# Kernel tuning notes

Measured on AMD Instinct MI355X. Metric: run time of the kernel, lower is better.

## Reference

```python
import jax, jax.numpy as jnp
import numpy as np

B, N, C, K = 2, 8192, 128, 16

def _mlp2(h, W1, b1, W2, b2):
    return jax.nn.relu(h @ W1 + b1) @ W2 + b2

def setup_inputs() -> dict:
    key = jax.random.key(0)
    ks = jax.random.split(key, 20)
    s = lambda d: 1.0 / np.sqrt(d)
    inp = {
        "x": jax.random.normal(ks[0], (B, N, C), jnp.float32),
        "position": jax.random.normal(ks[1], (B, N, 3), jnp.float32),
        "Wq": jax.random.normal(ks[2], (C, C), jnp.float32) * s(C),
        "bq": jnp.zeros((C,), jnp.float32),
        "Wk": jax.random.normal(ks[3], (C, C), jnp.float32) * s(C),
        "bk": jnp.zeros((C,), jnp.float32),
        "Wv": jax.random.normal(ks[4], (C, C), jnp.float32) * s(C),
        "bv": jnp.zeros((C,), jnp.float32),
        "Wp1": jax.random.normal(ks[5], (3, C), jnp.float32) * s(3),
        "bp1": jnp.zeros((C,), jnp.float32),
        "Wp2": jax.random.normal(ks[6], (C, C), jnp.float32) * s(C),
        "bp2": jnp.zeros((C,), jnp.float32),
        "Wg1": jax.random.normal(ks[7], (C, C), jnp.float32) * s(C),
        "bg1": jnp.zeros((C,), jnp.float32),
        "Wg2": jax.random.normal(ks[8], (C, C), jnp.float32) * s(C),
        "bg2": jnp.zeros((C,), jnp.float32),
    }
    return inp

def reference(x, position, Wq, bq, Wk, bk, Wv, bv, Wp1, bp1, Wp2, bp2, Wg1, bg1, Wg2, bg2):
    # kNN via squared pairwise distances (monotone in cdist, same topk indices)
    p2 = jnp.sum(position * position, axis=-1)                       # (B,N)
    d2 = p2[:, :, None] + p2[:, None, :] - 2.0 * jnp.einsum("bnd,bmd->bnm", position, position)
    _, idx = jax.lax.top_k(-d2, K)                                    # (B,N,K) nearest (incl self)

    gather = jax.vmap(lambda arr, i: arr[i])                          # per-batch fancy gather
    neighbors = gather(x, idx)                                        # (B,N,K,C)
    pos_nb = gather(position, idx)                                    # (B,N,K,3)

    q = x @ Wq + bq                                                   # (B,N,C)
    k = neighbors @ Wk + bk                                           # (B,N,K,C)
    v = neighbors @ Wv + bv                                           # (B,N,K,C)

    # positional MLP only at gathered pairs (same math as all-pairs-then-gather)
    rel = position[:, :, None, :] - pos_nb                            # (B,N,K,3)
    pe = _mlp2(rel, Wp1, bp1, Wp2, bp2)                               # (B,N,K,C)

    scale = 1.0 / jnp.sqrt(jnp.float32(C))
    attn = (q[:, :, None, :] - k + pe) * scale
    attn = _mlp2(attn, Wg1, bg1, Wg2, bg2)
    attn = jax.nn.softmax(attn, axis=2)                               # softmax over K neighbors
    out = jnp.sum(attn * (v + pe), axis=2)                            # (B,N,C)
    return out
```

## Files before the change

kernel.cpp:

```cpp
#include <hip/hip_runtime.h>
#include <hip/hip_bf16.h>
#include <stdint.h>

#define NPTS 8192
#define CDIM 128
#define KNNK 16
#define WELEMF 16384
#define SCALE 0.08838834764831845f
#define FLDS_BYTES 74752
#define GRES 16
#define NCELL (GRES*GRES*GRES)

typedef __attribute__((ext_vector_type(4))) float f32x4;
typedef __attribute__((ext_vector_type(8))) short s16x8;

__device__ __forceinline__ unsigned short to_bf16(float f){
  union { __hip_bfloat16 h; unsigned short u; } v;
  v.h = __float2bfloat16(f);
  return v.u;
}

__device__ __forceinline__ s16x8 cvt8(const float* p){
  float4 lo = *(const float4*)p;
  float4 hi = *(const float4*)(p + 4);
  s16x8 f;
  f[0]=(short)to_bf16(lo.x); f[1]=(short)to_bf16(lo.y);
  f[2]=(short)to_bf16(lo.z); f[3]=(short)to_bf16(lo.w);
  f[4]=(short)to_bf16(hi.x); f[5]=(short)to_bf16(hi.y);
  f[6]=(short)to_bf16(hi.z); f[7]=(short)to_bf16(hi.w);
  return f;
}

__device__ __forceinline__ unsigned mapf_u(unsigned s){
  return s ^ (0x80000000u | (unsigned)(((int)s) >> 31));
}
__device__ __forceinline__ float unmapf_u(unsigned u){
  unsigned r = (u & 0x80000000u) ? (u ^ 0x80000000u) : ~u;
  return __uint_as_float(r);
}

__global__ __launch_bounds__(256) void zero_init_kernel(int* __restrict__ counts,
                                                        unsigned* __restrict__ bbox)
{
  int t = blockIdx.x*256 + threadIdx.x;
  if (t < 2*NCELL) counts[t] = 0;
  if (t < 12) bbox[t] = ((t % 6) < 3) ? 0xFFFFFFFFu : 0u;
}

__global__ __launch_bounds__(256) void prep_kernel(
    const float* __restrict__ Wq, const float* __restrict__ Wk,
    const float* __restrict__ Wv, const float* __restrict__ Wp2,
    const float* __restrict__ Wg1, const float* __restrict__ Wg2,
    const float* __restrict__ pos,
    unsigned short* __restrict__ wt, float4* __restrict__ pos4,
    unsigned* __restrict__ bbox)
{
  int t = blockIdx.x*256 + threadIdx.x;
  if (t < 6*WELEMF){
    int w = t >> 14, f = t & (WELEMF-1);
    int i = f & 7, ln = (f >> 3) & 63, kkct = f >> 9;
    int kk = kkct & 3, ct = kkct >> 2;
    int kdim = kk*32 + (ln >> 4)*8 + i, col = ct*16 + (ln & 15);
    const float* src = (w==0)?Wq:(w==1)?Wk:(w==2)?Wv:(w==3)?Wp2:(w==4)?Wg1:Wg2;
    float v = src[kdim*CDIM + col];
    if (w == 1) v = -v;
    wt[t] = to_bf16(v);
  } else {
    int m = t - 6*WELEMF;
    float xx = pos[m*3+0], yy = pos[m*3+1], zz = pos[m*3+2];
    float p2 = __fadd_rn(__fadd_rn(__fmul_rn(xx,xx), __fmul_rn(yy,yy)), __fmul_rn(zz,zz));
    pos4[m] = make_float4(xx, yy, zz, p2);
    unsigned mnx = mapf_u(__float_as_uint(xx)), mny = mapf_u(__float_as_uint(yy)), mnz = mapf_u(__float_as_uint(zz));
    unsigned mxx = mnx, mxy = mny, mxz = mnz;
#pragma unroll
    for (int off = 1; off < 64; off <<= 1){
      mnx = min(mnx, (unsigned)__shfl_xor((int)mnx, off));
      mny = min(mny, (unsigned)__shfl_xor((int)mny, off));
      mnz = min(mnz, (unsigned)__shfl_xor((int)mnz, off));
      mxx = max(mxx, (unsigned)__shfl_xor((int)mxx, off));
      mxy = max(mxy, (unsigned)__shfl_xor((int)mxy, off));
      mxz = max(mxz, (unsigned)__shfl_xor((int)mxz, off));
    }
    if ((threadIdx.x & 63) == 0){
      int b = m >> 13;
      atomicMin(&bbox[b*6+0], mnx); atomicMin(&bbox[b*6+1], mny); atomicMin(&bbox[b*6+2], mnz);
      atomicMax(&bbox[b*6+3], mxx); atomicMax(&bbox[b*6+4], mxy); atomicMax(&bbox[b*6+5], mxz);
    }
  }
}

__global__ __launch_bounds__(256) void bin_count_kernel(
    const float4* __restrict__ pos4, const unsigned* __restrict__ bbox,
    int* __restrict__ counts, int* __restrict__ cellId)
{
  int m = blockIdx.x*256 + threadIdx.x;
  int b = m >> 13;
  float4 p = pos4[m];
  float lox = unmapf_u(bbox[b*6+0]), loy = unmapf_u(bbox[b*6+1]), loz = unmapf_u(bbox[b*6+2]);
  float hix = unmapf_u(bbox[b*6+3]), hiy = unmapf_u(bbox[b*6+4]), hiz = unmapf_u(bbox[b*6+5]);
  int ix = min(GRES-1, max(0, (int)((p.x - lox) * ((float)GRES/(hix-lox)))));
  int iy = min(GRES-1, max(0, (int)((p.y - loy) * ((float)GRES/(hiy-loy)))));
  int iz = min(GRES-1, max(0, (int)((p.z - loz) * ((float)GRES/(hiz-loz)))));
  int cid = (iz*GRES + iy)*GRES + ix;
  cellId[m] = cid;
  atomicAdd(&counts[b*NCELL + cid], 1);
}

__global__ __launch_bounds__(1024) void scan_kernel(
    const int* __restrict__ counts, int* __restrict__ starts, int* __restrict__ cursor)
{
  __shared__ int part[1024];
  int b = blockIdx.x, t = threadIdx.x;
  const int* c = counts + b*NCELL;
  int* s = starts + b*(NCELL+1);
  int* cur = cursor + b*NCELL;
  int base = t*4, sum = 0;
  for (int i = 0; i < 4; ++i) sum += c[base+i];
  part[t] = sum; __syncthreads();
  for (int off = 1; off < 1024; off <<= 1){
    int v = (t >= off) ? part[t-off] : 0;
    __syncthreads();
    part[t] += v;
    __syncthreads();
  }
  int run = (t > 0) ? part[t-1] : 0;
  for (int i = 0; i < 4; ++i){ int cc = c[base+i]; s[base+i] = run; cur[base+i] = run; run += cc; }
  if (t == 1023) s[NCELL] = run;
}

__global__ __launch_bounds__(256) void scatter_kernel(
    const float4* __restrict__ pos4, const int* __restrict__ cellId,
    int* __restrict__ cursor, float4* __restrict__ spos4)
{
  int m = blockIdx.x*256 + threadIdx.x;
  int b = m >> 13;
  float4 p = pos4[m];
  int dst = atomicAdd(&cursor[b*NCELL + cellId[m]], 1);
  spos4[(b<<13) + dst] = make_float4(p.x, p.y, p.z, __uint_as_float((unsigned)(m & (NPTS-1))));
}

__global__ __launch_bounds__(256) void knn_grid_kernel(
    const float4* __restrict__ spos4, const int* __restrict__ starts,
    const unsigned* __restrict__ bbox, int* __restrict__ idxout)
{
  const int tid = threadIdx.x, lane = tid & 63;
  const int g = blockIdx.x*4 + (tid >> 6);
  const int b = g >> 13, n = g & (NPTS-1);
  const float4* sp = spos4 + ((size_t)b<<13);
  const int*    st = starts + b*(NCELL+1);

  const float4 q4 = sp[n];
  const int orig = __float_as_int(q4.w);
  const float qx = q4.x, qy = q4.y, qz = q4.z;
  const float q2 = __fadd_rn(__fadd_rn(__fmul_rn(qx,qx), __fmul_rn(qy,qy)), __fmul_rn(qz,qz));

  float lox = unmapf_u(bbox[b*6+0]), loy = unmapf_u(bbox[b*6+1]), loz = unmapf_u(bbox[b*6+2]);
  float hix = unmapf_u(bbox[b*6+3]), hiy = unmapf_u(bbox[b*6+4]), hiz = unmapf_u(bbox[b*6+5]);
  float cwx = (hix-lox)*(1.0f/GRES), cwy = (hiy-loy)*(1.0f/GRES), cwz = (hiz-loz)*(1.0f/GRES);
  int cx = min(GRES-1, max(0, (int)((qx - lox) * ((float)GRES/(hix-lox)))));
  int cy = min(GRES-1, max(0, (int)((qy - loy) * ((float)GRES/(hiy-loy)))));
  int cz = min(GRES-1, max(0, (int)((qz - loz) * ((float)GRES/(hiz-loz)))));

  unsigned khi = 0xFFFFFFFFu, klo = 0xFFFFFFFFu;
  float Tf = __builtin_inff();

  auto insert = [&](unsigned ihi, unsigned ilo){
    unsigned phi = (unsigned)__builtin_amdgcn_update_dpp(0, (int)khi, 0x111, 0xF, 0xF, false);
    unsigned plo = (unsigned)__builtin_amdgcn_update_dpp(0, (int)klo, 0x111, 0xF, 0xF, false);
    bool gt  = (khi > ihi) || (khi == ihi && klo > ilo);
    bool pgt = ((lane & 15) != 0) && ((phi > ihi) || (phi == ihi && plo > ilo));
    khi = gt ? (pgt ? phi : ihi) : khi;
    klo = gt ? (pgt ? plo : ilo) : klo;
  };
  auto updT = [&](){
    unsigned t15 = (unsigned)__builtin_amdgcn_readlane((int)khi, 15);
    Tf = (t15 >= 0xFF800000u) ? __builtin_inff() : unmapf_u(t15);
  };

  for (int R = 1; R <= GRES-1; ++R){
    const bool first = (R == 1);
    const int per = 8*R, w1 = 2*R-1;
    const int ntask = first ? 9 : (per + 2*w1*w1);
    for (int tb = 0; tb < ntask; tb += 64){
      int t = tb + lane;
      int dy = 0, dz = 0, gx0 = 0, gx1 = -1;
      bool valid = t < ntask;
      if (first){
        if (valid){ dy = t % 3 - 1; dz = t / 3 - 1; }
        gx0 = max(cx-1, 0); gx1 = min(cx+1, GRES-1);
      } else if (valid){
        if (t < per){
          int s2 = 2*(2*R+1);
          if (t < s2){ dz = (t < 2*R+1) ? -R : R; dy = t % (2*R+1) - R; }
          else { int u = t - s2; dy = (u & 1) ? R : -R; dz = (u >> 1) - (R-1); }
          gx0 = max(cx-R, 0); gx1 = min(cx+R, GRES-1);
        } else {
          int i = t - per, ri = i >> 1;
          dy = ri % w1 - (R-1); dz = ri / w1 - (R-1);
          int gx = cx + ((i & 1) ? R : -R);
          gx0 = gx; gx1 = gx;
          valid = gx >= 0 && gx <= GRES-1;
        }
      }
      int gy = cy + dy, gz = cz + dz;
      valid = valid && gy >= 0 && gy < GRES && gz >= 0 && gz < GRES && gx0 <= gx1;
      int s0 = 0, s1 = 0;
      if (valid){ int cb = (gz*GRES + gy)*GRES; s0 = st[cb + gx0]; s1 = st[cb + gx1 + 1]; }
      unsigned long long cm = __ballot(valid && (s1 > s0));
      while (cm){
        int sl = (int)__builtin_ctzll(cm); cm &= cm - 1;
        int cs = __builtin_amdgcn_readlane(s0, sl);
        int ce = __builtin_amdgcn_readlane(s1, sl);
        for (int p0 = cs; p0 < ce; p0 += 64){
          int mm = p0 + lane;
          bool v = mm < ce;
          float4 c = v ? sp[mm] : make_float4(0.f,0.f,0.f,0.f);
          float c2  = __fadd_rn(__fadd_rn(__fmul_rn(c.x,c.x), __fmul_rn(c.y,c.y)), __fmul_rn(c.z,c.z));
          float dot = __builtin_fmaf(c.z, qz, __builtin_fmaf(c.y, qy, __fmul_rn(c.x, qx)));
          float d2  = __fsub_rn(__fadd_rn(q2, c2), __fadd_rn(dot, dot));
          int oi = __float_as_int(c.w);
          bool ins = v && (d2 <= Tf);
          unsigned long long im = __ballot(ins);
          if (im){
            while (im){
              int s = (int)__builtin_ctzll(im); im &= im - 1;
              unsigned dvb = (unsigned)__builtin_amdgcn_readlane((int)__float_as_uint(d2), s);
              int ov = __builtin_amdgcn_readlane(oi, s);
              insert(mapf_u(dvb), (unsigned)ov);
            }
            updT();
          }
        }
      }
    }
    const float big = 1e30f;
    float dxlo = (cx-R <= 0)      ? big : (qx - (lox + (float)(cx-R)*cwx));
    float dxhi = (cx+R >= GRES-1) ? big : ((lox + (float)(cx+R+1)*cwx) - qx);
    float dylo = (cy-R <= 0)      ? big : (qy - (loy + (float)(cy-R)*cwy));
    float dyhi = (cy+R >= GRES-1) ? big : ((loy + (float)(cy+R+1)*cwy) - qy);
    float dzlo = (cz-R <= 0)      ? big : (qz - (loz + (float)(cz-R)*cwz));
    float dzhi = (cz+R >= GRES-1) ? big : ((loz + (float)(cz+R+1)*cwz) - qz);
    float dmin = fminf(fminf(fminf(dxlo,dxhi), fminf(dylo,dyhi)), fminf(dzlo,dzhi));
    if (dmin >= 1e29f) break;
    dmin = fmaxf(dmin, 0.0f);
    float dmin2 = dmin*dmin;
    if (Tf + 1e-4f + Tf*1e-5f < dmin2) break;
  }
  if (lane < KNNK) idxout[(((size_t)b<<13) + orig)*KNNK + lane] = (int)klo;
}

__global__ __launch_bounds__(256, 2) void fused_kernel(
    const float* __restrict__ x, const float* __restrict__ pos,
    const float* __restrict__ bq, const float* __restrict__ bk,
    const float* __restrict__ bv, const float* __restrict__ Wp1,
    const float* __restrict__ bp1, const float* __restrict__ bp2,
    const float* __restrict__ bg1, const float* __restrict__ bg2,
    const int* __restrict__ idxws, const unsigned short* __restrict__ wt,
    float* __restrict__ out)
{
  extern __shared__ char smem[];
  char* Sbase = smem;
  char* Tbase = smem + 32768;
  float* blds = (float*)(smem + 65536);
  float* q_lds = (float*)(smem + 70656);

  const int tid = threadIdx.x;
  const int lane = tid & 63, w = tid >> 6;
  const int r = lane & 15, grp = lane >> 4;
  const int pbase = blockIdx.x * 8;
  const int b = pbase >> 13;

  auto gll = [&](int s, char* dst){
#pragma unroll
    for (int k = 0; k < 8; ++k){
      int c = w*8 + k;
      unsigned short* g = const_cast<unsigned short*>(wt) + (size_t)s*WELEMF + c*512 + lane*8;
      __builtin_amdgcn_global_load_lds(
        (const __attribute__((address_space(1))) void*)g,
        (__attribute__((address_space(3))) void*)(dst + c*1024), 16, 0, 0);
    }
  };
  auto ldS = [&](int ct, int kk) -> s16x8 {
    return *(const s16x8*)&((unsigned short*)Sbase)[((ct*4 + kk)*64 + lane)*8];
  };
  auto ldT = [&](int ct, int kk) -> s16x8 {
    return *(const s16x8*)&((unsigned short*)Tbase)[((ct*4 + kk)*64 + lane)*8];
  };

  gll(0, Sbase);
  gll(3, Tbase);

  for (int e = tid; e < 1280; e += 256){
    float v;
    if      (e < 128)  v = bq[e];
    else if (e < 256)  v = bk[e-128];
    else if (e < 384)  v = bv[e-256];
    else if (e < 512)  v = bp2[e-384];
    else if (e < 640)  v = bg1[e-512];
    else if (e < 768)  v = bg2[e-640];
    else if (e < 896)  v = bp1[e-768];
    else               v = Wp1[e-896];
    blds[e] = v;
  }
  int nbr[2]; float relx[2], rely[2], relz[2];
#pragma unroll
  for (int j = 0; j < 2; ++j){
    int gp = pbase + w*2 + j;
    nbr[j] = idxws[(size_t)gp*KNNK + r];
    const float* pq = pos + (size_t)gp*3;
    const float* pn = pos + ((size_t)b*NPTS + nbr[j])*3;
    relx[j] = pq[0]-pn[0]; rely[j] = pq[1]-pn[1]; relz[j] = pq[2]-pn[2];
  }
  s16x8 qa[4];
  {
    const float* xr = x + (size_t)(pbase + (r & 7))*CDIM;
#pragma unroll
    for (int kk = 0; kk < 4; ++kk) qa[kk] = cvt8(xr + kk*32 + grp*8);
  }
  __syncthreads();

  {
    f32x4 qacc[2] = { {0.f,0.f,0.f,0.f}, {0.f,0.f,0.f,0.f} };
#pragma unroll
    for (int c2 = 0; c2 < 2; ++c2){
      int ct = w*2 + c2;
#pragma unroll
      for (int kk = 0; kk < 4; ++kk)
        qacc[c2] = __builtin_amdgcn_mfma_f32_16x16x32_bf16(qa[kk], ldS(ct,kk), qacc[c2], 0,0,0);
    }
#pragma unroll
    for (int c2 = 0; c2 < 2; ++c2){
      int col = (w*2+c2)*16 + r;
#pragma unroll
      for (int jj = 0; jj < 4; ++jj){
        int row = grp*4 + jj;
        if (row < 8) q_lds[row*CDIM + col] = qacc[c2][jj] + blds[col];
      }
    }
  }
  s16x8 pf[2][4];
#pragma unroll
  for (int j = 0; j < 2; ++j)
#pragma unroll
    for (int kk = 0; kk < 4; ++kk){
      s16x8 f;
#pragma unroll
      for (int i = 0; i < 8; ++i){
        int kc = kk*32 + grp*8 + i;
        float s = relx[j]*blds[896+kc] + rely[j]*blds[1024+kc] + relz[j]*blds[1152+kc] + blds[768+kc];
        f[i] = (short)to_bf16(fmaxf(s, 0.f));
      }
      pf[j][kk] = f;
    }
  __syncthreads();
  gll(1, Sbase);

  f32x4 at[2][8], av[2][8];
#pragma unroll
  for (int j=0;j<2;++j)
#pragma unroll
    for (int ct=0;ct<8;++ct) at[j][ct] = (f32x4){0.f,0.f,0.f,0.f};
#pragma unroll
  for (int ct=0;ct<8;++ct)
#pragma unroll
    for (int kk=0;kk<4;++kk){
      s16x8 bw = ldT(ct,kk);
#pragma unroll
      for (int j=0;j<2;++j)
        at[j][ct] = __builtin_amdgcn_mfma_f32_16x16x32_bf16(pf[j][kk], bw, at[j][ct], 0,0,0);
    }
  s16x8 nf[2][4];
#pragma unroll
  for (int j=0;j<2;++j)
#pragma unroll
    for (int kk=0;kk<4;++kk)
      nf[j][kk] = cvt8(x + ((size_t)b*NPTS + nbr[j])*CDIM + kk*32 + grp*8);

  __syncthreads();
  gll(2, Tbase);
#pragma unroll
  for (int j=0;j<2;++j)
#pragma unroll
    for (int ct=0;ct<8;++ct) av[j][ct] = at[j][ct];
#pragma unroll
  for (int ct=0;ct<8;++ct)
#pragma unroll
    for (int kk=0;kk<4;++kk){
      s16x8 bw = ldS(ct,kk);
#pragma unroll
      for (int j=0;j<2;++j) at[j][ct] = __builtin_amdgcn_mfma_f32_16x16x32_bf16(nf[j][kk], bw, at[j][ct], 0,0,0);
    }
  __syncthreads();
  gll(4, Sbase);
#pragma unroll
  for (int ct=0;ct<8;++ct)
#pragma unroll
    for (int kk=0;kk<4;++kk){
      s16x8 bw = ldT(ct,kk);
#pragma unroll
      for (int j=0;j<2;++j) av[j][ct] = __builtin_amdgcn_mfma_f32_16x16x32_bf16(nf[j][kk], bw, av[j][ct], 0,0,0);
    }
#pragma unroll
  for (int j=0;j<2;++j){
    int prow = (w*2+j)*CDIM;
#pragma unroll
    for (int ct=0;ct<8;++ct){
      int col = ct*16+r;
      float add = q_lds[prow+col] + blds[384+col] - blds[128+col];
#pragma unroll
      for (int jj=0;jj<4;++jj) at[j][ct][jj] = (at[j][ct][jj] + add)*SCALE;
    }
  }
  __syncthreads();

#pragma unroll
  for (int j=0;j<2;++j){
    unsigned short* tj = (unsigned short*)Tbase + (w*2+j)*2048;
#pragma unroll
    for (int ct=0;ct<8;++ct){
      int base = (ct>>1)*512 + ((ct&1)*2 + (r>>3))*128 + (r&7);
#pragma unroll
      for (int jj=0;jj<4;++jj)
        tj[base + (grp*4+jj)*8] = to_bf16(at[j][ct][jj]);
    }
  }
  s16x8 tf[2][4];
#pragma unroll
  for (int j=0;j<2;++j){
    const unsigned short* tj = (const unsigned short*)Tbase + (w*2+j)*2048;
#pragma unroll
    for (int kk=0;kk<4;++kk)
      tf[j][kk] = *(const s16x8*)&tj[(kk*64 + lane)*8];
  }
  f32x4 hacc[2][8];
#pragma unroll
  for (int j=0;j<2;++j)
#pragma unroll
    for (int ct=0;ct<8;++ct) hacc[j][ct] = (f32x4){0.f,0.f,0.f,0.f};
#pragma unroll
  for (int ct=0;ct<8;++ct)
#pragma unroll
    for (int kk=0;kk<4;++kk){
      s16x8 bw = ldS(ct,kk);
#pragma unroll
      for (int j=0;j<2;++j)
        hacc[j][ct] = __builtin_amdgcn_mfma_f32_16x16x32_bf16(tf[j][kk], bw, hacc[j][ct], 0,0,0);
    }
  __syncthreads();
  gll(5, Sbase);
#pragma unroll
  for (int j=0;j<2;++j){
    unsigned short* tj = (unsigned short*)Tbase + (w*2+j)*2048;
#pragma unroll
    for (int ct=0;ct<8;++ct){
      int base = (ct>>1)*512 + ((ct&1)*2 + (r>>3))*128 + (r&7);
      int col = ct*16+r; float bb = blds[512+col];
#pragma unroll
      for (int jj=0;jj<4;++jj)
        tj[base + (grp*4+jj)*8] = to_bf16(fmaxf(hacc[j][ct][jj]+bb, 0.f));
    }
  }
  s16x8 hf[2][4];
#pragma unroll
  for (int j=0;j<2;++j){
    const unsigned short* tj = (const unsigned short*)Tbase + (w*2+j)*2048;
#pragma unroll
    for (int kk=0;kk<4;++kk)
      hf[j][kk] = *(const s16x8*)&tj[(kk*64 + lane)*8];
  }
  __syncthreads();
  f32x4 gacc[2][8];
#pragma unroll
  for (int j=0;j<2;++j)
#pragma unroll
    for (int ct=0;ct<8;++ct) gacc[j][ct] = (f32x4){0.f,0.f,0.f,0.f};
#pragma unroll
  for (int ct=0;ct<8;++ct)
#pragma unroll
    for (int kk=0;kk<4;++kk){
      s16x8 bw = ldS(ct,kk);
#pragma unroll
      for (int j=0;j<2;++j)
        gacc[j][ct] = __builtin_amdgcn_mfma_f32_16x16x32_bf16(hf[j][kk], bw, gacc[j][ct], 0,0,0);
    }
#pragma unroll
  for (int j=0;j<2;++j){
#pragma unroll
    for (int ct=0;ct<8;++ct){
      int col = ct*16+r;
      float gb = blds[640+col];
      float g0v = gacc[j][ct][0]+gb, g1v = gacc[j][ct][1]+gb;
      float g2v = gacc[j][ct][2]+gb, g3v = gacc[j][ct][3]+gb;
      float mx = fmaxf(fmaxf(g0v,g1v), fmaxf(g2v,g3v));
      mx = fmaxf(mx, __shfl_xor(mx,16));
      mx = fmaxf(mx, __shfl_xor(mx,32));
      float e0=__expf(g0v-mx), e1=__expf(g1v-mx), e2=__expf(g2v-mx), e3=__expf(g3v-mx);
      float vb = blds[256+col] + blds[384+col];
      float ss = e0+e1+e2+e3;
      float oo = e0*(av[j][ct][0]+vb) + e1*(av[j][ct][1]+vb)
               + e2*(av[j][ct][2]+vb) + e3*(av[j][ct][3]+vb);
      ss += __shfl_xor(ss,16); ss += __shfl_xor(ss,32);
      oo += __shfl_xor(oo,16); oo += __shfl_xor(oo,32);
      if (grp == 0) out[(size_t)(pbase + w*2 + j)*CDIM + col] = oo/ss;
    }
  }
}

extern "C" void kernel_launch(void* const* d_in, const int* in_sizes, int n_in,
                              void* d_out, int out_size, void* d_ws, size_t ws_size,
                              hipStream_t stream)
{
  const float* x    = (const float*)d_in[0];
  const float* pos  = (const float*)d_in[1];
  const float* Wq   = (const float*)d_in[2];
  const float* bq   = (const float*)d_in[3];
  const float* Wk   = (const float*)d_in[4];
  const float* bk   = (const float*)d_in[5];
  const float* Wv   = (const float*)d_in[6];
  const float* bv   = (const float*)d_in[7];
  const float* Wp1  = (const float*)d_in[8];
  const float* bp1  = (const float*)d_in[9];
  const float* Wp2  = (const float*)d_in[10];
  const float* bp2  = (const float*)d_in[11];
  const float* Wg1  = (const float*)d_in[12];
  const float* bg1  = (const float*)d_in[13];
  const float* Wg2  = (const float*)d_in[14];
  const float* bg2  = (const float*)d_in[15];
  float* out = (float*)d_out;

  char* ws = (char*)d_ws;
  int*            idxs   = (int*)ws;
  unsigned short* wt     = (unsigned short*)(ws + 1048576);
  float4*         pos4   = (float4*)(ws + 1257472);
  float4*         spos4  = (float4*)(ws + 1519616);
  int*            cellId = (int*)(ws + 1847296);
  int*            counts = (int*)(ws + 1912832);
  int*            starts = (int*)(ws + 2174976);
  int*            cursor = (int*)(ws + 2437376);
  unsigned*       bbox   = (unsigned*)(ws + 2699520);

  hipFuncSetAttribute((const void*)fused_kernel,
                      hipFuncAttributeMaxDynamicSharedMemorySize, FLDS_BYTES);

  zero_init_kernel<<<32, 256, 0, stream>>>(counts, bbox);
  prep_kernel<<<448, 256, 0, stream>>>(Wq, Wk, Wv, Wp2, Wg1, Wg2, pos, wt, pos4, bbox);
  bin_count_kernel<<<64, 256, 0, stream>>>(pos4, bbox, counts, cellId);
  scan_kernel<<<2, 1024, 0, stream>>>(counts, starts, cursor);
  scatter_kernel<<<64, 256, 0, stream>>>(pos4, cellId, cursor, spos4);
  knn_grid_kernel<<<4096, 256, 0, stream>>>(spos4, starts, bbox, idxs);
  fused_kernel<<<2048, 256, FLDS_BYTES, stream>>>(x, pos, bq, bk, bv, Wp1, bp1, bp2,
                                                  bg1, bg2, idxs, wt, out);
}
```

Baseline: 219.1 us.

## Process four kNN queries per wavefront using 16-lane subgroups

The grid kNN kernel now handles four query points per 64-lane wavefront, each on a 16-lane subgroup, instead of one query per wavefront. Ballots are masked per subgroup, readlane becomes shuffles, and the wave exits only once every subgroup has finished its search. Launched blocks drop by four times. This targets the many idle lanes in scans of small cells and in the serial insert loop, but adds divergence between subgroups whose searches differ in length, and each subgroup scans candidates only 16 at a time.

After: 211.4 us. 3.5% less time.

```diff
diff --git a/kernel.cpp b/kernel.cpp
--- a/kernel.cpp
+++ b/kernel.cpp
@@ -144,7 +144,9 @@
     const unsigned* __restrict__ bbox, int* __restrict__ idxout)
 {
   const int tid = threadIdx.x, lane = tid & 63;
-  const int g = blockIdx.x*4 + (tid >> 6);
+  const int sub = lane >> 4, sl = lane & 15, gbase = sub*16;
+  const int w = tid >> 6;
+  const int g = blockIdx.x*16 + w*4 + sub;
   const int b = g >> 13, n = g & (NPTS-1);
   const float4* sp = spos4 + ((size_t)b<<13);
   const int*    st = starts + b*(NCELL+1);
@@ -168,23 +170,24 @@
     unsigned phi = (unsigned)__builtin_amdgcn_update_dpp(0, (int)khi, 0x111, 0xF, 0xF, false);
     unsigned plo = (unsigned)__builtin_amdgcn_update_dpp(0, (int)klo, 0x111, 0xF, 0xF, false);
     bool gt  = (khi > ihi) || (khi == ihi && klo > ilo);
-    bool pgt = ((lane & 15) != 0) && ((phi > ihi) || (phi == ihi && plo > ilo));
+    bool pgt = (sl != 0) && ((phi > ihi) || (phi == ihi && plo > ilo));
     khi = gt ? (pgt ? phi : ihi) : khi;
     klo = gt ? (pgt ? plo : ilo) : klo;
   };
   auto updT = [&](){
-    unsigned t15 = (unsigned)__builtin_amdgcn_readlane((int)khi, 15);
+    unsigned t15 = (unsigned)__shfl((int)khi, gbase + 15);
     Tf = (t15 >= 0xFF800000u) ? __builtin_inff() : unmapf_u(t15);
   };
 
+  bool gdone = false;
   for (int R = 1; R <= GRES-1; ++R){
     const bool first = (R == 1);
     const int per = 8*R, w1 = 2*R-1;
     const int ntask = first ? 9 : (per + 2*w1*w1);
-    for (int tb = 0; tb < ntask; tb += 64){
-      int t = tb + lane;
+    for (int tb = 0; tb < ntask; tb += 16){
+      int t = tb + sl;
       int dy = 0, dz = 0, gx0 = 0, gx1 = -1;
-      bool valid = t < ntask;
+      bool valid = (!gdone) && (t < ntask);
       if (first){
         if (valid){ dy = t % 3 - 1; dz = t / 3 - 1; }
         gx0 = max(cx-1, 0); gx1 = min(cx+1, GRES-1);
@@ -206,13 +209,17 @@
       valid = valid && gy >= 0 && gy < GRES && gz >= 0 && gz < GRES && gx0 <= gx1;
       int s0 = 0, s1 = 0;
       if (valid){ int cb = (gz*GRES + gy)*GRES; s0 = st[cb + gx0]; s1 = st[cb + gx1 + 1]; }
-      unsigned long long cm = __ballot(valid && (s1 > s0));
-      while (cm){
-        int sl = (int)__builtin_ctzll(cm); cm &= cm - 1;
-        int cs = __builtin_amdgcn_readlane(s0, sl);
-        int ce = __builtin_amdgcn_readlane(s1, sl);
-        for (int p0 = cs; p0 < ce; p0 += 64){
-          int mm = p0 + lane;
+      unsigned long long bal = __ballot(valid && (s1 > s0));
+      unsigned cm = (unsigned)((bal >> gbase) & 0xFFFFull);
+      while (__any(cm != 0)){
+        bool act = (cm != 0);
+        int srow = act ? __builtin_ctz(cm) : 0;
+        if (act) cm &= cm - 1;
+        int cs = __shfl(s0, gbase + srow);
+        int ce = __shfl(s1, gbase + srow);
+        if (!act){ cs = 0; ce = 0; }
+        for (int p0 = cs; p0 < ce; p0 += 16){
+          int mm = p0 + sl;
           bool v = mm < ce;
           float4 c = v ? sp[mm] : make_float4(0.f,0.f,0.f,0.f);
           float c2  = __fadd_rn(__fadd_rn(__fmul_rn(c.x,c.x), __fmul_rn(c.y,c.y)), __fmul_rn(c.z,c.z));
@@ -220,13 +227,16 @@
           float d2  = __fsub_rn(__fadd_rn(q2, c2), __fadd_rn(dot, dot));
           int oi = __float_as_int(c.w);
           bool ins = v && (d2 <= Tf);
-          unsigned long long im = __ballot(ins);
-          if (im){
-            while (im){
-              int s = (int)__builtin_ctzll(im); im &= im - 1;
-              unsigned dvb = (unsigned)__builtin_amdgcn_readlane((int)__float_as_uint(d2), s);
-              int ov = __builtin_amdgcn_readlane(oi, s);
-              insert(mapf_u(dvb), (unsigned)ov);
+          unsigned long long ib = __ballot(ins);
+          unsigned im = (unsigned)((ib >> gbase) & 0xFFFFull);
+          if (__any(im != 0)){
+            while (__any(im != 0)){
+              bool a2 = (im != 0);
+              int s = a2 ? __builtin_ctz(im) : 0;
+              if (a2) im &= im - 1;
+              unsigned dvb = (unsigned)__shfl((int)__float_as_uint(d2), gbase + s);
+              int ov = __shfl(oi, gbase + s);
+              if (a2) insert(mapf_u(dvb), (unsigned)ov);
             }
             updT();
           }
@@ -241,12 +251,14 @@
     float dzlo = (cz-R <= 0)      ? big : (qz - (loz + (float)(cz-R)*cwz));
     float dzhi = (cz+R >= GRES-1) ? big : ((loz + (float)(cz+R+1)*cwz) - qz);
     float dmin = fminf(fminf(fminf(dxlo,dxhi), fminf(dylo,dyhi)), fminf(dzlo,dzhi));
-    if (dmin >= 1e29f) break;
+    bool full = dmin >= 1e29f;
     dmin = fmaxf(dmin, 0.0f);
     float dmin2 = dmin*dmin;
-    if (Tf + 1e-4f + Tf*1e-5f < dmin2) break;
-  }
-  if (lane < KNNK) idxout[(((size_t)b<<13) + orig)*KNNK + lane] = (int)klo;
+    bool stop = full || (Tf + 1e-4f + Tf*1e-5f < dmin2);
+    gdone = gdone || stop;
+    if (__all(gdone)) break;
+  }
+  idxout[(((size_t)b<<13) + orig)*KNNK + sl] = (int)klo;
 }
 
 __global__ __launch_bounds__(256, 2) void fused_kernel(
@@ -547,7 +559,7 @@
   bin_count_kernel<<<64, 256, 0, stream>>>(pos4, bbox, counts, cellId);
   scan_kernel<<<2, 1024, 0, stream>>>(counts, starts, cursor);
   scatter_kernel<<<64, 256, 0, stream>>>(pos4, cellId, cursor, spos4);
-  knn_grid_kernel<<<4096, 256, 0, stream>>>(spos4, starts, bbox, idxs);
+  knn_grid_kernel<<<1024, 256, 0, stream>>>(spos4, starts, bbox, idxs);
   fused_kernel<<<2048, 256, FLDS_BYTES, stream>>>(x, pos, bq, bk, bv, Wp1, bp1, bp2,
                                                   bg1, bg2, idxs, wt, out);
 }
```
